# Optimization experiments

Hardware: AMD Instinct MI355X
Metric: run time of the kernel (lower is better)

The kernel has to match this reference:

```python
import jax, jax.numpy as jnp
import numpy as np

LN_EPS = 1e-5
NRM_EPS = 1e-12


def layernorm(x, w, b):
    mu = x.mean(-1, keepdims=True)
    var = ((x - mu) ** 2).mean(-1, keepdims=True)
    return (x - mu) * jax.lax.rsqrt(var + LN_EPS) * w + b


def cdist(x, y):
    # Euclidean pairwise distance over trailing (N, C): (..., N, C) x (..., M, C) -> (..., N, M)
    x2 = (x * x).sum(-1)
    y2 = (y * y).sum(-1)
    xy = jnp.einsum('...ic,...jc->...ij', x, y)
    return jnp.sqrt(jnp.maximum(x2[..., :, None] + y2[..., None, :] - 2.0 * xy, NRM_EPS))


def l2norm_last(x):
    n = jnp.sqrt((x * x).sum(-1, keepdims=True))
    return x / jnp.maximum(n, NRM_EPS)


def attn_qcs_sd(anchor, positive, neg1, neg2, k, alpha):
    # anchor/positive: (B,N,C); neg1/neg2: (2,B,N,C)
    # torch.tensor(neg) in the original detaches neg1/neg2 from autograd
    neg1 = jax.lax.stop_gradient(neg1)
    neg2 = jax.lax.stop_gradient(neg2)
    k = k + 1.0
    S_p = cdist(positive, anchor)           # (B,N,N)
    S_p = S_p - S_p.min()
    S_p = S_p.max() - S_p
    S_a = l2norm_last(S_p).sum(1)           # (B,N)
    S_p1 = l2norm_last(jnp.swapaxes(S_p, 1, 2)).sum(1)  # (B,N)

    def proc(D):  # (B,N,N) -> (B,N)
        D = D - D.min()
        return l2norm_last(D).sum(1)

    def pair(neg, tgt):  # neg (2,B,N,C), tgt (B,N,C)
        D = cdist(neg, jnp.broadcast_to(tgt[None], neg.shape))  # (2,B,N,N)
        return proc(D[0]), proc(D[1])

    d11, d12 = pair(neg1, anchor)
    d21, d22 = pair(neg2, anchor)
    map1 = S_a + k * ((d11 + d12) / 2 * alpha + (1 - alpha) * ((d21 + d22) / 2))
    d11, d12 = pair(neg1, positive)
    d21, d22 = pair(neg2, positive)
    map2 = S_p1 + k * ((d11 + d12) / 2 * alpha + (1 - alpha) * ((d21 + d22) / 2))
    return map1[..., None], map2[..., None]  # (B,N,1) each


def setup_inputs() -> dict:
    key = jax.random.key(0)
    B, N, C = 8, 1024, 768
    ks = jax.random.split(key, 12)
    s = 1.0 / np.sqrt(C)
    sh = 1.0 / np.sqrt(4 * C)
    return {
        'anchor': jax.random.normal(ks[0], (B, N, C), jnp.float32),
        'positive': jax.random.normal(ks[1], (B, N, C), jnp.float32),
        'neg1': jax.random.normal(ks[2], (2, B, N, C), jnp.float32),
        'neg2': jax.random.normal(ks[3], (2, B, N, C), jnp.float32),
        'norm1_w': jnp.ones((C,), jnp.float32),
        'norm1_b': jnp.zeros((C,), jnp.float32),
        'norm2_w': jnp.ones((C,), jnp.float32),
        'norm2_b': jnp.zeros((C,), jnp.float32),
        'proj_W': jax.random.uniform(ks[4], (C, 2 * C), jnp.float32, -s, s),
        'proj_b': jax.random.uniform(ks[5], (2 * C,), jnp.float32, -s, s),
        'fc1_W': jax.random.uniform(ks[6], (C, 4 * C), jnp.float32, -s, s),
        'fc1_b': jax.random.uniform(ks[7], (4 * C,), jnp.float32, -s, s),
        'fc2_W': jax.random.uniform(ks[8], (4 * C, C), jnp.float32, -sh, sh),
        'fc2_b': jax.random.uniform(ks[9], (C,), jnp.float32, -sh, sh),
        'theta': jnp.float32(0.0),
        'alpha': jnp.float32(0.0),
    }


def reference(anchor, positive, neg1, neg2, norm1_w, norm1_b, norm2_w, norm2_b,
              proj_W, proj_b, fc1_W, fc1_b, fc2_W, fc2_b, theta, alpha):
    def projsplit(x):
        y = x @ proj_W + proj_b
        C = x.shape[-1]
        return y[..., :C], y[..., C:]  # qk, v

    anc = layernorm(anchor, norm1_w, norm1_b)
    pos = layernorm(positive, norm1_w, norm1_b)
    n1 = layernorm(neg1, norm1_w, norm1_b)   # (2,B,N,C)
    n2 = layernorm(neg2, norm1_w, norm1_b)
    qk_x, v_x = projsplit(anc)
    qk_p, v_p = projsplit(pos)
    qk_n1, v_n1 = projsplit(n1)
    qk_n2, v_n2 = projsplit(n2)

    k = jnp.tanh(theta)
    al = jax.nn.sigmoid(alpha)

    a_a, a_p = attn_qcs_sd(qk_x, qk_p, qk_n1, qk_n2, k, al)
    n1_a, n1_p = attn_qcs_sd(qk_n1[0], qk_n1[1], jnp.stack([qk_x, qk_p]), qk_n2, k, al)
    n2_a, n2_p = attn_qcs_sd(qk_n2[0], qk_n2[1], jnp.stack([qk_x, qk_p]), qk_n1, k, al)

    anc_o = a_a * v_x + anc
    pos_o = a_p * v_p + pos
    neg1_o = jnp.stack([n1_a * v_n1[0] * n1[0], n1_p * v_n1[1] * n1[1]])
    neg2_o = jnp.stack([n2_a * v_n2[0] * n2[0], n2_p * v_n2[1] * n2[1]])

    def block(x):
        h = layernorm(x, norm2_w, norm2_b)
        h = jax.nn.gelu(h @ fc1_W + fc1_b, approximate=False) @ fc2_W + fc2_b
        return h + x

    return block(anc_o), block(pos_o), block(neg1_o), block(neg2_o)
```

## Files before the change

kernel.cpp:

```cpp
#include <hip/hip_runtime.h>
#include <hip/hip_bf16.h>


typedef short bshort8 __attribute__((ext_vector_type(8)));
typedef unsigned short u16x8 __attribute__((ext_vector_type(8)));
typedef float f32x4  __attribute__((ext_vector_type(4)));

#define AS1 __attribute__((address_space(1)))
#define AS3 __attribute__((address_space(3)))

#define B_   8
#define N_   1024
#define C_   768
#define MT   8192
#define M6   49152

#define OFF_QKNORM   0ull
#define OFF_MAPS     196608ull
#define OFF_STATS    393216ull
#define OFF_WBUF     2359296ull
#define OFF_MM       3342336ull
#define MEMSET_BYTES 3342464ull
#define OFF_WTPROJ   3342592ull
#define OFF_WTFC1    5701888ull
#define OFF_WTFC2    10420480ull
#define OFF_LNBF     15139072ull
#define OFF_QKBF     90636544ull
#define OFF_XHBF     OFF_QKBF
#define OFF_VBF      166134016ull
#define OFF_DBUF     241631488ull
#define OFF_H1BF     OFF_DBUF

__constant__ int cSU[15] = {1,3,5, 2,3,4,5, 2,3,4,5, 4,5,4,5};
__constant__ int cSV[15] = {0,2,4, 0,0,0,0, 1,1,1,1, 2,2,3,3};
__constant__ int cTA[15] = {0,0,0, 1,1,2,2, 1,1,2,2, 2,2,2,2};
__constant__ int cTB[15] = {0,0,0, 1,1,1,1, 1,1,1,1, 2,2,2,2};

__device__ __forceinline__ void gll16(const void* g, void* l) {
    __builtin_amdgcn_global_load_lds((const AS1 unsigned int*)g,
                                     (AS3 unsigned int*)l, 16, 0, 0);
}
__device__ __forceinline__ unsigned short f2bu(float v) {
    __hip_bfloat16 h = __float2bfloat16(v);
    return *reinterpret_cast<unsigned short*>(&h);
}
__device__ __forceinline__ float bu2f(unsigned short u) {
    __hip_bfloat16 h;
    *reinterpret_cast<unsigned short*>(&h) = u;
    return __bfloat162float(h);
}
__device__ __forceinline__ int xcd_swz(int flat, int nwg) {
    return (flat & 7) * (nwg >> 3) + (flat >> 3);
}

__device__ __forceinline__ void gemm256_core(const __hip_bfloat16* __restrict__ A,
                                             const __hip_bfloat16* __restrict__ Bt,
                                             int lda, int ldb, int kTiles,
                                             char* smem, f32x4 acc[8][4])
{
    const int tid = threadIdx.x;
    const int L   = tid & 63;
    const int m   = L & 15, q = L >> 4;
    const int w   = tid >> 6;
    const int wm  = w >> 2, wn = w & 3;

    const char* gA[4]; const char* gB[4];
    int lA[4], lB[4];
#pragma unroll
    for (int i = 0; i < 4; ++i) {
        int c  = tid + 512 * i;
        int r  = c >> 3;
        int gk = (c & 7) ^ (r & 7);
        gA[i] = (const char*)(A  + (size_t)r * lda) + gk * 16;
        gB[i] = (const char*)(Bt + (size_t)r * ldb) + gk * 16;
        lA[i] = c * 16;
        lB[i] = 32768 + c * 16;
    }
    const int aBase = wm * 16384 + m * 128;
    const int bBase = 32768 + wn * 8192 + m * 128;
    const int s0    = (q ^ (m & 7)) * 16;

    f32x4 z = {0.f, 0.f, 0.f, 0.f};
#pragma unroll
    for (int i = 0; i < 8; ++i)
#pragma unroll
        for (int j = 0; j < 4; ++j) acc[i][j] = z;

#pragma unroll
    for (int i = 0; i < 4; ++i) { gll16(gA[i], smem + lA[i]); gll16(gB[i], smem + lB[i]); }

    for (int kt = 0; kt < kTiles; ++kt) {
        __syncthreads();
        char* cur = smem + (kt & 1) * 65536;
        if (kt + 1 < kTiles) {
            char* nxt = smem + ((kt + 1) & 1) * 65536;
            const int adv = (kt + 1) * 128;
#pragma unroll
            for (int i = 0; i < 4; ++i) {
                gll16(gA[i] + adv, nxt + lA[i]);
                gll16(gB[i] + adv, nxt + lB[i]);
            }
        }
#pragma unroll
        for (int ks = 0; ks < 2; ++ks) {
            const int so = s0 ^ (ks * 64);
            bshort8 af[8], bf[4];
#pragma unroll
            for (int mi = 0; mi < 8; ++mi)
                af[mi] = *(const bshort8*)(cur + aBase + mi * 2048 + so);
#pragma unroll
            for (int nj = 0; nj < 4; ++nj)
                bf[nj] = *(const bshort8*)(cur + bBase + nj * 2048 + so);
#pragma unroll
            for (int mi = 0; mi < 8; ++mi)
#pragma unroll
                for (int nj = 0; nj < 4; ++nj)
                    acc[mi][nj] = __builtin_amdgcn_mfma_f32_16x16x32_bf16(af[mi], bf[nj], acc[mi][nj], 0, 0, 0);
        }
    }
}

__global__ __launch_bounds__(256) void transpose_conv(const float* __restrict__ in,
                                                      __hip_bfloat16* __restrict__ out,
                                                      int R, int C)
{
    __shared__ float tile[32][33];
    int bx = blockIdx.x * 32, by = blockIdx.y * 32;
    int tx = threadIdx.x, ty = threadIdx.y;
#pragma unroll
    for (int i = 0; i < 32; i += 8)
        tile[ty + i][tx] = in[(size_t)(by + ty + i) * C + bx + tx];
    __syncthreads();
#pragma unroll
    for (int i = 0; i < 32; i += 8)
        out[(size_t)(bx + ty + i) * R + by + tx] = __float2bfloat16(tile[tx][ty + i]);
}

__global__ void init_mm(unsigned int* mm)
{
    int i = threadIdx.x;
    if (i < 15) { mm[i] = 0x7f800000u; mm[15 + i] = 0u; }
}

__global__ __launch_bounds__(256) void ln1_kernel(const float* __restrict__ anchor,
                                                  const float* __restrict__ positive,
                                                  const float* __restrict__ neg1,
                                                  const float* __restrict__ neg2,
                                                  const float* __restrict__ w1,
                                                  const float* __restrict__ b1,
                                                  __hip_bfloat16* __restrict__ lnbf)
{
    int w = threadIdx.x >> 6, L = threadIdx.x & 63;
    int r = blockIdx.x * 4 + w;
    int t = r >> 13, within = r & 8191;
    const float* src;
    if      (t == 0) src = anchor   + (size_t)within * C_;
    else if (t == 1) src = positive + (size_t)within * C_;
    else if (t <  4) src = neg1 + ((size_t)(t - 2) * MT + within) * C_;
    else             src = neg2 + ((size_t)(t - 4) * MT + within) * C_;
    float4 x[3]; float s = 0.f, sq = 0.f;
#pragma unroll
    for (int j = 0; j < 3; ++j) {
        x[j] = *(const float4*)(src + 4 * L + 256 * j);
        s  += x[j].x + x[j].y + x[j].z + x[j].w;
        sq += x[j].x*x[j].x + x[j].y*x[j].y + x[j].z*x[j].z + x[j].w*x[j].w;
    }
#pragma unroll
    for (int o = 1; o < 64; o <<= 1) { s += __shfl_xor(s, o, 64); sq += __shfl_xor(sq, o, 64); }
    float mu  = s * (1.f / 768.f);
    float var = sq * (1.f / 768.f) - mu * mu;
    float rs  = rsqrtf(var + 1e-5f);
    __hip_bfloat16* dst = lnbf + (size_t)r * C_;
#pragma unroll
    for (int j = 0; j < 3; ++j) {
        int c = 4 * L + 256 * j;
        float4 wv = *(const float4*)(w1 + c);
        float4 bv = *(const float4*)(b1 + c);
        ushort4 o;
        o.x = f2bu((x[j].x - mu) * rs * wv.x + bv.x);
        o.y = f2bu((x[j].y - mu) * rs * wv.y + bv.y);
        o.z = f2bu((x[j].z - mu) * rs * wv.z + bv.z);
        o.w = f2bu((x[j].w - mu) * rs * wv.w + bv.w);
        *(ushort4*)(dst + c) = o;
    }
}

__global__ __launch_bounds__(512, 2) void gemm_proj(const __hip_bfloat16* __restrict__ A,
                                                    const __hip_bfloat16* __restrict__ Wt,
                                                    const float* __restrict__ bias,
                                                    __hip_bfloat16* __restrict__ qkbf,
                                                    __hip_bfloat16* __restrict__ vbf,
                                                    float* __restrict__ qknorm)
{
    __shared__ __align__(16) char smem[131072];
    int flat = blockIdx.x + 6 * blockIdx.y;
    int sf   = xcd_swz(flat, 6 * 192);
    int bx = sf % 6, by = sf / 6;
    f32x4 acc[8][4];
    gemm256_core(A + (size_t)by * 256 * C_, Wt + (size_t)bx * 256 * C_,
                 C_, C_, 12, smem, acc);
    int tid = threadIdx.x, w = tid >> 6, L = tid & 63, m = L & 15, q = L >> 4;
    int wm = w >> 2, wn = w & 3;
    int rowBase = by * 256 + wm * 128;
    int colBase = bx * 256 + wn * 64;
    bool isQK = (bx < 3);
    float bv[4];
#pragma unroll
    for (int nj = 0; nj < 4; ++nj) bv[nj] = bias[colBase + nj * 16 + m];
#pragma unroll
    for (int mi = 0; mi < 8; ++mi) {
#pragma unroll
        for (int r = 0; r < 4; ++r) {
            int row = rowBase + mi * 16 + 4 * q + r;
            float sqsum = 0.f;
#pragma unroll
            for (int nj = 0; nj < 4; ++nj) {
                int col = colBase + nj * 16 + m;
                float val = acc[mi][nj][r] + bv[nj];
                if (isQK) {
                    qkbf[(size_t)row * C_ + col] = __float2bfloat16(val);
                    sqsum += val * val;
                } else {
                    vbf[(size_t)row * C_ + (col - C_)] = __float2bfloat16(val);
                }
            }
            if (isQK) {
#pragma unroll
                for (int o = 1; o < 16; o <<= 1) sqsum += __shfl_xor(sqsum, o, 64);
                if (m == 0) atomicAdd(qknorm + row, sqsum);
            }
        }
    }
}

__global__ __launch_bounds__(512, 2) void gram_kernel(const __hip_bfloat16* __restrict__ qkbf,
                                                      const float* __restrict__ qknorm,
                                                      __hip_bfloat16* __restrict__ Dbuf,
                                                      float* __restrict__ stats,
                                                      unsigned int* __restrict__ mm,
                                                      int sb)
{
    __shared__ __align__(16) char smem[131072];
    int flat = blockIdx.x + 16 * blockIdx.y + 128 * blockIdx.z;
    int nwg  = 128 * gridDim.z;
    int sf   = xcd_swz(flat, nwg);
    int tile = sf & 15;
    int b    = (sf >> 4) & 7;
    int z    = sf >> 7;
    int slab = sb + z;
    int TI = tile >> 2, TJ = tile & 3;
    int u = cSU[slab], v = cSV[slab];

    const __hip_bfloat16* Ab = qkbf + (size_t)(u * MT + b * N_ + TI * 256) * C_;
    const __hip_bfloat16* Bb = qkbf + (size_t)(v * MT + b * N_ + TJ * 256) * C_;
    f32x4 acc[8][4];
    gemm256_core(Ab, Bb, C_, C_, 12, smem, acc);

    int tid = threadIdx.x, w = tid >> 6, L = tid & 63, m = L & 15, q = L >> 4;
    int wm = w >> 2, wn = w & 3;
    int rowBase = TI * 256 + wm * 128;
    int colBase = TJ * 256 + wn * 64;
    const float* nu = qknorm + u * MT + b * N_;
    const float* nv = qknorm + v * MT + b * N_;
    float nbv[4];
#pragma unroll
    for (int nj = 0; nj < 4; ++nj) nbv[nj] = nv[colBase + nj * 16 + m];

    unsigned short* Dz = (unsigned short*)Dbuf + (size_t)z * 8388608ull + ((size_t)b << 20);
    int tile128 = (TI * 2 + wm) * 8 + TJ * 2 + (wn >> 1);
    float* rs1 = stats + (size_t)slab * 32768;
    float* rs2 = rs1 + 8192;
    float* cs1 = rs1 + 16384;
    float* cs2 = rs1 + 24576;

    float dmin = 3.0e38f, dmax = 0.f;
    float col1[4] = {0.f,0.f,0.f,0.f}, col2[4] = {0.f,0.f,0.f,0.f};
#pragma unroll
    for (int mi = 0; mi < 8; ++mi) {
        float na[4];
#pragma unroll
        for (int r = 0; r < 4; ++r) na[r] = nu[rowBase + mi * 16 + 4 * q + r];
        float dv[4][4];
        float h1v[4] = {0.f,0.f,0.f,0.f}, h2v[4] = {0.f,0.f,0.f,0.f};
#pragma unroll
        for (int nj = 0; nj < 4; ++nj) {
#pragma unroll
            for (int r = 0; r < 4; ++r) {
                float d = sqrtf(fmaxf(na[r] + nbv[nj] - 2.f * acc[mi][nj][r], 1e-12f));
                dv[nj][r] = d;
                h1v[r] += d; h2v[r] += d * d;
                col1[nj] += d; col2[nj] += d * d;
                dmin = fminf(dmin, d); dmax = fmaxf(dmax, d);
            }
        }
        unsigned short* base = Dz + (size_t)tile128 * 16384
                             + (((mi >> 2) << 1) | (wn & 1)) * 4096
                             + ((mi & 3) * 2) * 512 + m * 32 + q * 8;
#pragma unroll
        for (int tp = 0; tp < 2; ++tp) {
            u16x8 pk;
#pragma unroll
            for (int e = 0; e < 8; ++e)
                pk[e] = f2bu(dv[2 * tp + (e >> 2)][e & 3]);
            *(u16x8*)(base + tp * 512) = pk;
        }
#pragma unroll
        for (int r = 0; r < 4; ++r) {
            float h1 = h1v[r], h2 = h2v[r];
#pragma unroll
            for (int o = 1; o < 16; o <<= 1) { h1 += __shfl_xor(h1, o, 64); h2 += __shfl_xor(h2, o, 64); }
            if (m == 0) {
                int row = rowBase + mi * 16 + 4 * q + r;
                atomicAdd(rs1 + b * N_ + row, h1);
                atomicAdd(rs2 + b * N_ + row, h2);
            }
        }
    }
#pragma unroll
    for (int nj = 0; nj < 4; ++nj) {
        float c1 = col1[nj], c2 = col2[nj];
        c1 += __shfl_xor(c1, 16, 64); c1 += __shfl_xor(c1, 32, 64);
        c2 += __shfl_xor(c2, 16, 64); c2 += __shfl_xor(c2, 32, 64);
        if (q == 0) {
            int col = colBase + nj * 16 + m;
            atomicAdd(cs1 + b * N_ + col, c1);
            atomicAdd(cs2 + b * N_ + col, c2);
        }
    }
#pragma unroll
    for (int o = 1; o < 64; o <<= 1) {
        dmin = fminf(dmin, __shfl_xor(dmin, o, 64));
        dmax = fmaxf(dmax, __shfl_xor(dmax, o, 64));
    }
    if (L == 0) {
        atomicMin(mm + slab, __float_as_uint(dmin));
        atomicMax(mm + 15 + slab, __float_as_uint(dmax));
    }
}

__global__ __launch_bounds__(256) void weights_kernel(const float* __restrict__ stats,
                                                      const unsigned int* __restrict__ mm,
                                                      float* __restrict__ wbuf,
                                                      float* __restrict__ maps,
                                                      const float* __restrict__ theta,
                                                      const float* __restrict__ alpha,
                                                      int sb)
{
    int job = blockIdx.x, b = blockIdx.y;
    int slab = sb + (job >> 1);
    int useB = job & 1;
    const float* s1 = stats + (size_t)slab * 32768 + useB * 16384;
    const float* s2 = s1 + 8192;
    int type = useB ? cTB[slab] : cTA[slab];
    int dst  = useB ? cSU[slab] : cSV[slab];
    float off = (type == 0) ? __uint_as_float(mm[15 + slab]) : __uint_as_float(mm[slab]);
    float k  = tanhf(theta[0]) + 1.0f;
    float al = 1.0f / (1.0f + expf(-alpha[0]));
    float cf = (type == 0) ? -1.0f : ((type == 1) ? 0.5f * k * al : 0.5f * k * (1.0f - al));
    float* wout = wbuf + (size_t)slab * 16384 + useB * 8192 + b * N_;

    float sumw = 0.f;
    for (int i = threadIdx.x; i < N_; i += 256) {
        float a1 = s1[b * N_ + i], a2 = s2[b * N_ + i];
        float nrm2  = fmaxf(a2 - 2.f * off * a1 + (float)N_ * off * off, 0.f);
        float denom = fmaxf(sqrtf(nrm2), 1e-12f);
        float wv = cf / denom;
        wout[i] = wv;
        sumw += wv;
    }
    int w = threadIdx.x >> 6, L = threadIdx.x & 63;
#pragma unroll
    for (int o = 1; o < 64; o <<= 1) sumw += __shfl_xor(sumw, o, 64);
    __shared__ float red[4];
    if (L == 0) red[w] = sumw;
    __syncthreads();
    float tot = red[0] + red[1] + red[2] + red[3];
    float Cb = -off * tot;
    for (int j = threadIdx.x; j < N_; j += 256)
        atomicAdd(maps + (size_t)dst * MT + b * N_ + j, Cb);
}

__global__ __launch_bounds__(256) void wsum_kernel(const __hip_bfloat16* __restrict__ Dbuf,
                                                   const float* __restrict__ wbuf,
                                                   float* __restrict__ maps,
                                                   int sb)
{
    int z = blockIdx.z, slab = sb + z, b = blockIdx.y;
    int tile = blockIdx.x;
    int ti = tile >> 3, tj = tile & 7;
    int u = cSU[slab], v = cSV[slab];
    int tid = threadIdx.x, w = tid >> 6, L = tid & 63, m = L & 15, q = L >> 4;
    const unsigned short* Dc = (const unsigned short*)Dbuf + (size_t)z * 8388608ull
                               + ((size_t)b << 20) + (size_t)tile * 16384 + w * 4096;
    const float* wr = wbuf + (size_t)slab * 16384 + b * N_ + ti * 128;
    const float* wc = wbuf + (size_t)slab * 16384 + 8192 + b * N_ + tj * 128;

    __shared__ float swr[128], swc[128];
    if (threadIdx.x < 128) swr[threadIdx.x] = wr[threadIdx.x];
    else                   swc[threadIdx.x - 128] = wc[threadIdx.x - 128];
    __syncthreads();

    int wrbase = (w >> 1) * 64, wcbase = (w & 1) * 64;
    float wc1[4];
#pragma unroll
    for (int t = 0; t < 4; ++t) wc1[t] = swc[wcbase + 16 * t + m];
    float wr4[4][4];
#pragma unroll
    for (int s = 0; s < 4; ++s)
#pragma unroll
        for (int r = 0; r < 4; ++r) wr4[s][r] = swr[wrbase + 16 * s + 4 * q + r];

    float rowacc[4][4];
#pragma unroll
    for (int s = 0; s < 4; ++s)
#pragma unroll
        for (int r = 0; r < 4; ++r) rowacc[s][r] = 0.f;
    float colacc[4] = {0.f,0.f,0.f,0.f};

#pragma unroll
    for (int s = 0; s < 4; ++s) {
#pragma unroll
        for (int tp = 0; tp < 2; ++tp) {
            u16x8 d8 = *(const u16x8*)(Dc + (s * 2 + tp) * 512 + m * 32 + q * 8);
#pragma unroll
            for (int e = 0; e < 8; ++e) {
                int t = 2 * tp + (e >> 2), r = e & 3;
                float d = bu2f(d8[e]);
                rowacc[s][r] += wc1[t] * d;
                colacc[t]    += wr4[s][r] * d;
            }
        }
    }
#pragma unroll
    for (int s = 0; s < 4; ++s)
#pragma unroll
        for (int r = 0; r < 4; ++r) {
            float h = rowacc[s][r];
#pragma unroll
            for (int o = 1; o < 16; o <<= 1) h += __shfl_xor(h, o, 64);
            if (m == 0)
                atomicAdd(maps + (size_t)u * MT + b * N_ + ti * 128 + wrbase + 16 * s + 4 * q + r, h);
        }
#pragma unroll
    for (int t = 0; t < 4; ++t) {
        float c = colacc[t];
        c += __shfl_xor(c, 16, 64); c += __shfl_xor(c, 32, 64);
        if (q == 0)
            atomicAdd(maps + (size_t)v * MT + b * N_ + tj * 128 + wcbase + 16 * t + m, c);
    }
}

__global__ __launch_bounds__(256) void combine_ln2(const float* __restrict__ maps,
                                                   const __hip_bfloat16* __restrict__ vbf,
                                                   const __hip_bfloat16* __restrict__ lnbf,
                                                   const float* __restrict__ w2,
                                                   const float* __restrict__ b2,
                                                   float* __restrict__ dout,
                                                   __hip_bfloat16* __restrict__ xhbf)
{
    int w = threadIdx.x >> 6, L = threadIdx.x & 63;
    int r = blockIdx.x * 4 + w;
    int t = r >> 13;
    float mv = maps[r];
    const __hip_bfloat16* vp = vbf + (size_t)r * C_;
    const __hip_bfloat16* lp = lnbf + (size_t)r * C_;
    float x[12]; float s = 0.f, sq = 0.f;
#pragma unroll
    for (int j = 0; j < 3; ++j) {
        int c = 4 * L + 256 * j;
        ushort4 vv = *(const ushort4*)(vp + c);
        ushort4 ll = *(const ushort4*)(lp + c);
        float xv[4];
        xv[0] = (t < 2) ? (mv * bu2f(vv.x) + bu2f(ll.x)) : (mv * bu2f(vv.x) * bu2f(ll.x));
        xv[1] = (t < 2) ? (mv * bu2f(vv.y) + bu2f(ll.y)) : (mv * bu2f(vv.y) * bu2f(ll.y));
        xv[2] = (t < 2) ? (mv * bu2f(vv.z) + bu2f(ll.z)) : (mv * bu2f(vv.z) * bu2f(ll.z));
        xv[3] = (t < 2) ? (mv * bu2f(vv.w) + bu2f(ll.w)) : (mv * bu2f(vv.w) * bu2f(ll.w));
        float4 xo = {xv[0], xv[1], xv[2], xv[3]};
        *(float4*)(dout + (size_t)r * C_ + c) = xo;
#pragma unroll
        for (int e = 0; e < 4; ++e) { x[4*j+e] = xv[e]; s += xv[e]; sq += xv[e]*xv[e]; }
    }
#pragma unroll
    for (int o = 1; o < 64; o <<= 1) { s += __shfl_xor(s, o, 64); sq += __shfl_xor(sq, o, 64); }
    float mu  = s * (1.f / 768.f);
    float var = sq * (1.f / 768.f) - mu * mu;
    float rs  = rsqrtf(var + 1e-5f);
    __hip_bfloat16* dst = xhbf + (size_t)r * C_;
#pragma unroll
    for (int j = 0; j < 3; ++j) {
        int c = 4 * L + 256 * j;
        float4 wv = *(const float4*)(w2 + c);
        float4 bv = *(const float4*)(b2 + c);
        ushort4 o;
        o.x = f2bu((x[4*j+0] - mu) * rs * wv.x + bv.x);
        o.y = f2bu((x[4*j+1] - mu) * rs * wv.y + bv.y);
        o.z = f2bu((x[4*j+2] - mu) * rs * wv.z + bv.z);
        o.w = f2bu((x[4*j+3] - mu) * rs * wv.w + bv.w);
        *(ushort4*)(dst + c) = o;
    }
}

__global__ __launch_bounds__(512, 2) void gemm_ffn1(const __hip_bfloat16* __restrict__ A,
                                                    const __hip_bfloat16* __restrict__ Wt,
                                                    const float* __restrict__ bias,
                                                    __hip_bfloat16* __restrict__ h1)
{
    __shared__ __align__(16) char smem[131072];
    int flat = blockIdx.x + 12 * blockIdx.y;
    int sf   = xcd_swz(flat, 12 * 96);
    int bx = sf % 12, by = sf / 12;
    f32x4 acc[8][4];
    gemm256_core(A + (size_t)by * 256 * C_, Wt + (size_t)bx * 256 * C_,
                 C_, C_, 12, smem, acc);
    int tid = threadIdx.x, w = tid >> 6, L = tid & 63, m = L & 15, q = L >> 4;
    int wm = w >> 2, wn = w & 3;
    int rowBase = by * 256 + wm * 128;
    int colBase = bx * 256 + wn * 64;
    float bv[4];
#pragma unroll
    for (int nj = 0; nj < 4; ++nj) bv[nj] = bias[colBase + nj * 16 + m];
#pragma unroll
    for (int mi = 0; mi < 8; ++mi)
#pragma unroll
        for (int r = 0; r < 4; ++r) {
            int row = rowBase + mi * 16 + 4 * q + r;
#pragma unroll
            for (int nj = 0; nj < 4; ++nj) {
                int col = colBase + nj * 16 + m;
                float val = acc[mi][nj][r] + bv[nj];
                float ge  = 0.5f * val * (1.0f + erff(val * 0.70710678118654752f));
                h1[(size_t)row * 3072 + col] = __float2bfloat16(ge);
            }
        }
}

__global__ __launch_bounds__(512, 2) void gemm_ffn2(const __hip_bfloat16* __restrict__ A,
                                                    const __hip_bfloat16* __restrict__ Wt,
                                                    const float* __restrict__ bias,
                                                    float* __restrict__ out)
{
    __shared__ __align__(16) char smem[131072];
    int flat = blockIdx.x + 3 * blockIdx.y;
    int sf   = xcd_swz(flat, 3 * 96);
    int bx = sf % 3, by = sf / 3;
    f32x4 acc[8][4];
    gemm256_core(A + (size_t)by * 256 * 3072, Wt + (size_t)bx * 256 * 3072,
                 3072, 3072, 48, smem, acc);
    int tid = threadIdx.x, w = tid >> 6, L = tid & 63, m = L & 15, q = L >> 4;
    int wm = w >> 2, wn = w & 3;
    int rowBase = by * 256 + wm * 128;
    int colBase = bx * 256 + wn * 64;
    float bv[4];
#pragma unroll
    for (int nj = 0; nj < 4; ++nj) bv[nj] = bias[colBase + nj * 16 + m];
#pragma unroll
    for (int mi = 0; mi < 8; ++mi)
#pragma unroll
        for (int r = 0; r < 4; ++r) {
            int row = rowBase + mi * 16 + 4 * q + r;
#pragma unroll
            for (int nj = 0; nj < 4; ++nj) {
                int col = colBase + nj * 16 + m;
                size_t idx = (size_t)row * C_ + col;
                out[idx] = out[idx] + acc[mi][nj][r] + bv[nj];
            }
        }
}

extern "C" void kernel_launch(void* const* d_in, const int* in_sizes, int n_in,
                              void* d_out, int out_size, void* d_ws, size_t ws_size,
                              hipStream_t stream)
{
    (void)in_sizes; (void)n_in; (void)out_size; (void)ws_size;
    const float* anchor   = (const float*)d_in[0];
    const float* positive = (const float*)d_in[1];
    const float* neg1     = (const float*)d_in[2];
    const float* neg2     = (const float*)d_in[3];
    const float* n1w      = (const float*)d_in[4];
    const float* n1b      = (const float*)d_in[5];
    const float* n2w      = (const float*)d_in[6];
    const float* n2b      = (const float*)d_in[7];
    const float* projW    = (const float*)d_in[8];
    const float* projb    = (const float*)d_in[9];
    const float* fc1W     = (const float*)d_in[10];
    const float* fc1b     = (const float*)d_in[11];
    const float* fc2W     = (const float*)d_in[12];
    const float* fc2b     = (const float*)d_in[13];
    const float* theta    = (const float*)d_in[14];
    const float* alpha    = (const float*)d_in[15];
    float* dout = (float*)d_out;

    char* ws = (char*)d_ws;
    float*          qknorm = (float*)(ws + OFF_QKNORM);
    float*          maps   = (float*)(ws + OFF_MAPS);
    float*          stats  = (float*)(ws + OFF_STATS);
    float*          wbuf   = (float*)(ws + OFF_WBUF);
    unsigned int*   mm     = (unsigned int*)(ws + OFF_MM);
    __hip_bfloat16* WtProj = (__hip_bfloat16*)(ws + OFF_WTPROJ);
    __hip_bfloat16* WtFc1  = (__hip_bfloat16*)(ws + OFF_WTFC1);
    __hip_bfloat16* WtFc2  = (__hip_bfloat16*)(ws + OFF_WTFC2);
    __hip_bfloat16* lnbf   = (__hip_bfloat16*)(ws + OFF_LNBF);
    __hip_bfloat16* qkbf   = (__hip_bfloat16*)(ws + OFF_QKBF);
    __hip_bfloat16* xhbf   = (__hip_bfloat16*)(ws + OFF_XHBF);
    __hip_bfloat16* vbf    = (__hip_bfloat16*)(ws + OFF_VBF);
    __hip_bfloat16* Dbuf   = (__hip_bfloat16*)(ws + OFF_DBUF);
    __hip_bfloat16* h1bf   = (__hip_bfloat16*)(ws + OFF_H1BF);

    hipMemsetAsync(ws, 0, MEMSET_BYTES, stream);
    init_mm<<<1, 64, 0, stream>>>(mm);

    transpose_conv<<<dim3(48, 24), dim3(32, 8), 0, stream>>>(projW, WtProj, 768, 1536);
    transpose_conv<<<dim3(96, 24), dim3(32, 8), 0, stream>>>(fc1W,  WtFc1,  768, 3072);
    transpose_conv<<<dim3(24, 96), dim3(32, 8), 0, stream>>>(fc2W,  WtFc2,  3072, 768);

    ln1_kernel<<<12288, 256, 0, stream>>>(anchor, positive, neg1, neg2, n1w, n1b, lnbf);

    gemm_proj<<<dim3(6, 192), 512, 0, stream>>>(lnbf, WtProj, projb, qkbf, vbf, qknorm);

    for (int g = 0; g < 2; ++g) {
        int sb = g * 8;
        int ns = g ? 7 : 8;
        gram_kernel<<<dim3(16, 8, ns), 512, 0, stream>>>(qkbf, qknorm, Dbuf, stats, mm, sb);
        weights_kernel<<<dim3(2 * ns, 8), 256, 0, stream>>>(stats, mm, wbuf, maps, theta, alpha, sb);
        wsum_kernel<<<dim3(64, 8, ns), 256, 0, stream>>>(Dbuf, wbuf, maps, sb);
    }

    combine_ln2<<<12288, 256, 0, stream>>>(maps, vbf, lnbf, n2w, n2b, dout, xhbf);

    for (int ch = 0; ch < 2; ++ch) {
        size_t ro = (size_t)ch * 24576;
        gemm_ffn1<<<dim3(12, 96), 512, 0, stream>>>(xhbf + ro * C_, WtFc1, fc1b, h1bf);
        gemm_ffn2<<<dim3(3, 96), 512, 0, stream>>>(h1bf, WtFc2, fc2b, dout + ro * C_);
    }
}
```

Baseline: 1.720 ms.

## Prefetch two k-tiles ahead with explicit vmcnt waits in GEMM mainloop

Measured after the change: 1.747 ms. No clear change (+1.6%).

```diff
diff --git a/kernel.cpp b/kernel.cpp
--- a/kernel.cpp
+++ b/kernel.cpp
@@ -88,35 +88,57 @@
 
 #pragma unroll
     for (int i = 0; i < 4; ++i) { gll16(gA[i], smem + lA[i]); gll16(gB[i], smem + lB[i]); }
+#pragma unroll
+    for (int i = 0; i < 4; ++i) {
+        gll16(gA[i] + 128, smem + 65536 + lA[i]);
+        gll16(gB[i] + 128, smem + 65536 + lB[i]);
+    }
 
     for (int kt = 0; kt < kTiles; ++kt) {
-        __syncthreads();
+        if (kt + 1 < kTiles) asm volatile("s_waitcnt vmcnt(8)" ::: "memory");
+        else                 asm volatile("s_waitcnt vmcnt(0)" ::: "memory");
+        __builtin_amdgcn_s_barrier();
         char* cur = smem + (kt & 1) * 65536;
-        if (kt + 1 < kTiles) {
-            char* nxt = smem + ((kt + 1) & 1) * 65536;
-            const int adv = (kt + 1) * 128;
+
+        bshort8 af0[8], bf0[4], af1[8], bf1[4];
+        const int so0 = s0, so1 = s0 ^ 64;
+#pragma unroll
+        for (int mi = 0; mi < 8; ++mi)
+            af0[mi] = *(const bshort8*)(cur + aBase + mi * 2048 + so0);
+#pragma unroll
+        for (int nj = 0; nj < 4; ++nj)
+            bf0[nj] = *(const bshort8*)(cur + bBase + nj * 2048 + so0);
+#pragma unroll
+        for (int mi = 0; mi < 8; ++mi)
+            af1[mi] = *(const bshort8*)(cur + aBase + mi * 2048 + so1);
+#pragma unroll
+        for (int nj = 0; nj < 4; ++nj)
+            bf1[nj] = *(const bshort8*)(cur + bBase + nj * 2048 + so1);
+
+        asm volatile("s_waitcnt lgkmcnt(0)" ::: "memory");
+        __builtin_amdgcn_s_barrier();
+
+        if (kt + 2 < kTiles) {
+            const int adv = (kt + 2) * 128;
 #pragma unroll
             for (int i = 0; i < 4; ++i) {
-                gll16(gA[i] + adv, nxt + lA[i]);
-                gll16(gB[i] + adv, nxt + lB[i]);
-            }
-        }
-#pragma unroll
-        for (int ks = 0; ks < 2; ++ks) {
-            const int so = s0 ^ (ks * 64);
-            bshort8 af[8], bf[4];
-#pragma unroll
-            for (int mi = 0; mi < 8; ++mi)
-                af[mi] = *(const bshort8*)(cur + aBase + mi * 2048 + so);
+                gll16(gA[i] + adv, cur + lA[i]);
+                gll16(gB[i] + adv, cur + lB[i]);
+            }
+        }
+
+        __builtin_amdgcn_s_setprio(1);
+#pragma unroll
+        for (int mi = 0; mi < 8; ++mi)
 #pragma unroll
             for (int nj = 0; nj < 4; ++nj)
-                bf[nj] = *(const bshort8*)(cur + bBase + nj * 2048 + so);
-#pragma unroll
-            for (int mi = 0; mi < 8; ++mi)
-#pragma unroll
-                for (int nj = 0; nj < 4; ++nj)
-                    acc[mi][nj] = __builtin_amdgcn_mfma_f32_16x16x32_bf16(af[mi], bf[nj], acc[mi][nj], 0, 0, 0);
-        }
+                acc[mi][nj] = __builtin_amdgcn_mfma_f32_16x16x32_bf16(af0[mi], bf0[nj], acc[mi][nj], 0, 0, 0);
+#pragma unroll
+        for (int mi = 0; mi < 8; ++mi)
+#pragma unroll
+            for (int nj = 0; nj < 4; ++nj)
+                acc[mi][nj] = __builtin_amdgcn_mfma_f32_16x16x32_bf16(af1[mi], bf1[nj], acc[mi][nj], 0, 0, 0);
+        __builtin_amdgcn_s_setprio(0);
     }
 }
 
```
